# Performance work log

Hardware: AMD Instinct MI355X
Metric: run time of the kernel (lower is better)

## Reference

```python
import jax, jax.numpy as jnp
import numpy as np

N_NODES, N_EDGES, N_GRAPHS = 30000, 70000, 1024
TOWERS, F_IN, F_OUT, N_LAYERS = 5, 75, 15, 4
DEG_HIST = np.array([0.0, 100.0, 400.0, 300.0, 50.0], dtype=np.float32)
AVG_DEG_LOG = float((np.log(np.arange(len(DEG_HIST)) + 1.0) * DEG_HIST).sum() / DEG_HIST.sum())


def setup_inputs():
    key = jax.random.key(0)
    ks = jax.random.split(key, 16)
    g = lambda k, shp, fan: jax.random.normal(k, shp, jnp.float32) * (1.0 / np.sqrt(fan))
    return dict(
        x=jax.random.randint(ks[0], (N_NODES,), 0, 21),
        edge_index=jax.random.randint(ks[1], (2, N_EDGES), 0, N_NODES),
        edge_attr=jax.random.randint(ks[2], (N_EDGES,), 0, 4),
        batch=jnp.sort(jax.random.randint(ks[3], (N_NODES,), 0, N_GRAPHS)),
        node_emb=g(ks[4], (21, 75), 75),
        edge_emb=g(ks[5], (4, 50), 50),
        enc_w=g(ks[6], (N_LAYERS, 50, 75), 50),
        enc_b=jnp.zeros((N_LAYERS, 75), jnp.float32),
        pre_w=g(ks[7], (N_LAYERS, TOWERS, 3 * F_IN, F_IN), 3 * F_IN),
        pre_b=jnp.zeros((N_LAYERS, TOWERS, F_IN), jnp.float32),
        post_w=g(ks[8], (N_LAYERS, TOWERS, 13 * F_IN, F_OUT), 13 * F_IN),
        post_b=jnp.zeros((N_LAYERS, TOWERS, F_OUT), jnp.float32),
        lin_w=g(ks[9], (N_LAYERS, 75, 75), 75),
        lin_b=jnp.zeros((N_LAYERS, 75), jnp.float32),
        bn_g=jnp.ones((N_LAYERS, 75), jnp.float32),
        bn_b=jnp.zeros((N_LAYERS, 75), jnp.float32),
        mlp_w1=g(ks[10], (75, 50), 75), mlp_b1=jnp.zeros((50,), jnp.float32),
        mlp_w2=g(ks[11], (50, 25), 50), mlp_b2=jnp.zeros((25,), jnp.float32),
        mlp_w3=g(ks[12], (25, 1), 25), mlp_b3=jnp.zeros((1,), jnp.float32),
    )


def _pna_layer(h, src, dst, e_enc, pw, pb, qw, qb, lw, lb):
    n = h.shape[0]
    # message: cat[x_i, x_j, edge_enc] shared across towers, per-tower pre-NN
    msg = jnp.concatenate([h[dst], h[src], e_enc], axis=-1)            # [E, 3*F_in]
    m = jnp.einsum('ef,tfo->eto', msg, pw) + pb                        # [E, T, F_in]
    deg = jax.ops.segment_sum(jnp.ones((m.shape[0],), m.dtype), dst, n)
    has = (deg > 0)[:, None, None]
    cnt = jnp.maximum(deg, 1.0)[:, None, None]                         # clamp(1)
    mean = jax.ops.segment_sum(m, dst, n) / cnt
    mean_sq = jax.ops.segment_sum(m * m, dst, n) / cnt
    std = jnp.sqrt(jax.nn.relu(mean_sq - mean * mean) + 1e-5)
    mn = jnp.where(has, jax.ops.segment_min(m, dst, n), 0.0)
    mx = jnp.where(has, jax.ops.segment_max(m, dst, n), 0.0)
    agg = jnp.concatenate([mean, mn, mx, std], axis=-1)                # [N, T, 4*F_in]
    amp = jnp.log(cnt + 1.0) / AVG_DEG_LOG                             # amplification scaler
    scaled = jnp.concatenate([agg, agg * amp, agg / amp], axis=-1)     # [N, T, 12*F_in]
    post_in = jnp.concatenate(
        [jnp.broadcast_to(h[:, None, :], (n, TOWERS, F_IN)), scaled], axis=-1)  # [N, T, 13*F_in]
    out = jnp.einsum('ntf,tfo->nto', post_in, qw) + qb                 # [N, T, F_out]
    return out.reshape(n, TOWERS * F_OUT) @ lw + lb                    # [N, 75]


def _bn_relu(h, g, b):
    mu = h.mean(axis=0)
    var = h.var(axis=0)
    return jax.nn.relu((h - mu) * jax.lax.rsqrt(var + 1e-5) * g + b)


def reference(x, edge_index, edge_attr, batch, node_emb, edge_emb, enc_w, enc_b,
              pre_w, pre_b, post_w, post_b, lin_w, lin_b, bn_g, bn_b,
              mlp_w1, mlp_b1, mlp_w2, mlp_b2, mlp_w3, mlp_b3):
    h = node_emb[x]                      # [N, 75]
    e = edge_emb[edge_attr]              # [E, 50]
    src, dst = edge_index[0], edge_index[1]
    for l in range(N_LAYERS):
        e_enc = e @ enc_w[l] + enc_b[l]  # [E, 75]
        h = _bn_relu(_pna_layer(h, src, dst, e_enc, pre_w[l], pre_b[l],
                                post_w[l], post_b[l], lin_w[l], lin_b[l]),
                     bn_g[l], bn_b[l])
    hg = jax.ops.segment_sum(h, batch, N_GRAPHS)   # global_add_pool -> [G, 75]
    z = jax.nn.relu(hg @ mlp_w1 + mlp_b1)
    z = jax.nn.relu(z @ mlp_w2 + mlp_b2)
    return z @ mlp_w3 + mlp_b3
```

## Files before the change

### kernel.cpp

```cpp
#include <hip/hip_runtime.h>
#include <hip/hip_bf16.h>
#include <float.h>
#include <math.h>

#define NN 30000
#define NE 70000
#define NG 1024
#define NT 5
#define FI 75
#define NL 4

#define AMP_DENOM 1.1824939264481302f

#define ABW 832
#define AGW 1600
#define HBW 96
#define SBH 328

typedef __attribute__((ext_vector_type(8))) short bf16x8;
typedef __attribute__((ext_vector_type(4))) float f32x4;

__device__ __forceinline__ float bf2f(unsigned short u) {
    return __uint_as_float(((unsigned int)u) << 16);
}
__device__ __forceinline__ unsigned short f2bf(float f) {
    __hip_bfloat16 h = __float2bfloat16(f);
    return *reinterpret_cast<unsigned short*>(&h);
}

__global__ __launch_bounds__(256) void k_deg(const int* __restrict__ dst, int* __restrict__ deg) {
    int e = blockIdx.x * 256 + threadIdx.x;
    if (e < NE) atomicAdd(&deg[dst[e]], 1);
}

__global__ __launch_bounds__(1024) void k_scan(const int* __restrict__ deg, int* __restrict__ rowptr) {
    __shared__ int wsum[16];
    __shared__ int s_carry;
    int tid = threadIdx.x;
    int lane = tid & 63, wv = tid >> 6;
    if (tid == 0) s_carry = 0;
    __syncthreads();
    for (int base = 0; base < NN; base += 1024) {
        int i = base + tid;
        int v = (i < NN) ? deg[i] : 0;
        int x = v;
        #pragma unroll
        for (int off = 1; off < 64; off <<= 1) {
            int t = __shfl_up(x, off);
            if (lane >= off) x += t;
        }
        if (lane == 63) wsum[wv] = x;
        __syncthreads();
        if (tid < 16) {
            int y = wsum[tid];
            #pragma unroll
            for (int off = 1; off < 16; off <<= 1) {
                int t = __shfl_up(y, off);
                if (tid >= off) y += t;
            }
            wsum[tid] = y;
        }
        __syncthreads();
        int wbase = ((wv > 0) ? wsum[wv - 1] : 0) + s_carry;
        if (i < NN) rowptr[i] = wbase + x - v;
        int tot = wsum[15];
        __syncthreads();
        if (tid == 0) s_carry += tot;
    }
    __syncthreads();
    if (tid == 0) rowptr[NN] = s_carry;
}

__global__ __launch_bounds__(256) void k_scatter(const int* __restrict__ src, const int* __restrict__ dst,
                                                 const int* __restrict__ attr, const int* __restrict__ rowptr,
                                                 int* __restrict__ fill, int* __restrict__ csr) {
    int e = blockIdx.x * 256 + threadIdx.x;
    if (e < NE) {
        int d = dst[e];
        int pos = rowptr[d] + atomicAdd(&fill[d], 1);
        csr[pos] = src[e] | (attr[e] << 20);
    }
}

__global__ __launch_bounds__(256) void k_amp(const int* __restrict__ rowptr,
                                             float* __restrict__ amp, float* __restrict__ inv) {
    int n = blockIdx.x * 256 + threadIdx.x;
    if (n < NN) {
        int dg = rowptr[n + 1] - rowptr[n];
        float cnt = fmaxf((float)dg, 1.0f);
        float a = logf(cnt + 1.0f) * (1.0f / AMP_DENOM);
        amp[n] = a;
        inv[n] = 1.0f / a;
    }
}

__global__ __launch_bounds__(256) void k_h0(const int* __restrict__ x, const float* __restrict__ emb,
                                            float* __restrict__ h, unsigned short* __restrict__ hb) {
    int idx = blockIdx.x * 256 + threadIdx.x;
    if (idx < NN * HBW) {
        int n = idx / HBW, f = idx % HBW;
        if (f < FI) {
            float v = emb[x[n] * FI + f];
            h[n * FI + f] = v;
            hb[idx] = f2bf(v);
        } else {
            hb[idx] = 0;
        }
    }
}

__global__ __launch_bounds__(256) void k_wprep3(const float* __restrict__ post_w,
                                                unsigned short* __restrict__ Wpost2) {
    int idx = blockIdx.x * 256 + threadIdx.x;
    if (idx >= NL * NT * 3 * 16 * SBH) return;
    int kk = idx % SBH;
    int col = (idx / SBH) & 15;
    int s = (idx / (SBH * 16)) % 3;
    int t = (idx / (SBH * 16 * 3)) % NT;
    int l = idx / (SBH * 16 * 3 * NT);
    float val = 0.0f;
    if (kk < 304 && col < 15) {
        int stat = kk / 76, of = kk - stat * 76;
        if (of < 75)
            val = post_w[((size_t)(l * NT + t) * 975 + 75 + s * 300 + stat * 75 + of) * 15 + col];
    }
    Wpost2[idx] = f2bf(val);
}

__global__ __launch_bounds__(256) void k_wprep2(const float* __restrict__ pre_w,
                                                const float* __restrict__ post_w,
                                                unsigned short* __restrict__ WcatT) {
    int idx = blockIdx.x * 256 + threadIdx.x;
    if (idx >= NL * 832 * 96) return;
    int k = idx % 96;
    int j = (idx / 96) % 832;
    int l = idx / (96 * 832);
    float val = 0.0f;
    if (k < 75) {
        if (j < 375) {
            int t = j / 75, o = j % 75;
            val = pre_w[((size_t)(l * NT + t) * 225 + k) * FI + o];
        } else if (j < 750) {
            int jm = j - 375;
            int t = jm / 75, o = jm % 75;
            val = pre_w[((size_t)(l * NT + t) * 225 + 75 + k) * FI + o];
        } else if (j < 825) {
            int c = j - 750;
            int t = c / 15, o = c % 15;
            val = post_w[((size_t)(l * NT + t) * 975 + k) * 15 + o];
        }
    }
    WcatT[idx] = f2bf(val);
}

__global__ __launch_bounds__(384) void k_tbl(const float* __restrict__ edge_emb, const float* __restrict__ enc_w,
                                             const float* __restrict__ enc_b, const float* __restrict__ pre_w,
                                             const float* __restrict__ pre_b, int l,
                                             float* __restrict__ tbl, float* __restrict__ bnsum) {
    __shared__ float e4[4][FI];
    int tid = threadIdx.x;
    if (tid < 150) bnsum[tid] = 0.0f;
    if (tid < 300) {
        int a = tid / FI, f = tid % FI;
        float acc = enc_b[l * FI + f];
        for (int k = 0; k < 50; k++)
            acc += edge_emb[a * 50 + k] * enc_w[(l * 50 + k) * FI + f];
        e4[a][f] = acc;
    }
    __syncthreads();
    for (int idx = tid; idx < 4 * 375; idx += 384) {
        int a = idx / 375, c = idx % 375;
        int t = c / FI, o = c % FI;
        const float* wp = pre_w + ((size_t)(l * NT + t) * 225 + 150) * FI + o;
        float acc = pre_b[(l * NT + t) * FI + o];
        for (int f = 0; f < FI; f++)
            acc += e4[a][f] * wp[f * FI];
        tbl[idx] = acc;
    }
}

__global__ __launch_bounds__(256) void k_preab(const unsigned short* __restrict__ hb,
                                               const unsigned short* __restrict__ WcatT,
                                               int l, __hip_bfloat16* __restrict__ ABH) {
    __shared__ __align__(16) unsigned short sA[128 * 104];
    __shared__ __align__(16) unsigned short sB[208 * 104];
    int tid = threadIdx.x;
    int m0 = blockIdx.x * 128;
    int j0 = blockIdx.y * 208;

    const uint4* hsrc = (const uint4*)hb;
    for (int c = tid; c < 128 * 12; c += 256) {
        int r = c / 12, q = c % 12;
        int n = m0 + r;
        uint4 v = make_uint4(0, 0, 0, 0);
        if (n < NN) v = hsrc[(size_t)n * 12 + q];
        *(uint4*)&sA[r * 104 + q * 8] = v;
    }
    const uint4* wsrc = (const uint4*)(WcatT + (size_t)l * 832 * 96);
    for (int c = tid; c < 208 * 12; c += 256) {
        int r = c / 12, q = c % 12;
        *(uint4*)&sB[r * 104 + q * 8] = wsrc[(size_t)(j0 + r) * 12 + q];
    }
    __syncthreads();

    int w = tid >> 6, lane = tid & 63;
    int mw = w * 32;
    int lr = lane & 15, lq = lane >> 4;

    bf16x8 af[2][3];
    #pragma unroll
    for (int mt = 0; mt < 2; mt++)
        #pragma unroll
        for (int ks = 0; ks < 3; ks++)
            af[mt][ks] = *(const bf16x8*)&sA[(mw + mt * 16 + lr) * 104 + ks * 32 + lq * 8];

    f32x4 acc[13][2];
    #pragma unroll
    for (int nt = 0; nt < 13; nt++)
        #pragma unroll
        for (int mt = 0; mt < 2; mt++)
            acc[nt][mt] = (f32x4){0.0f, 0.0f, 0.0f, 0.0f};

    #pragma unroll
    for (int nt = 0; nt < 13; nt++) {
        #pragma unroll
        for (int ks = 0; ks < 3; ks++) {
            bf16x8 bf = *(const bf16x8*)&sB[(nt * 16 + lr) * 104 + ks * 32 + lq * 8];
            acc[nt][0] = __builtin_amdgcn_mfma_f32_16x16x32_bf16(af[0][ks], bf, acc[nt][0], 0, 0, 0);
            acc[nt][1] = __builtin_amdgcn_mfma_f32_16x16x32_bf16(af[1][ks], bf, acc[nt][1], 0, 0, 0);
        }
    }

    #pragma unroll
    for (int nt = 0; nt < 13; nt++) {
        int col = j0 + nt * 16 + lr;
        #pragma unroll
        for (int mt = 0; mt < 2; mt++) {
            #pragma unroll
            for (int r = 0; r < 4; r++) {
                int n = m0 + mw + mt * 16 + lq * 4 + r;
                if (n < NN) ABH[(size_t)n * ABW + col] = __float2bfloat16(acc[nt][mt][r]);
            }
        }
    }
}

__global__ __launch_bounds__(256) void k_gather(const __hip_bfloat16* __restrict__ ABH,
                                                const float* __restrict__ tbl,
                                                const int* __restrict__ rowptr, const int* __restrict__ csr,
                                                unsigned short* __restrict__ AGG) {
    __shared__ float s_tbl[1500];
    int tid = threadIdx.x;
    for (int i = tid; i < 1500; i += 256) s_tbl[i] = tbl[i];
    __syncthreads();

    int w = tid >> 6, l = tid & 63;
    int n = blockIdx.x * 4 + w;
    int base = rowptr[n];
    int dg = rowptr[n + 1] - base;

    float sum[6], ss[6], mn[6], mx[6];
    #pragma unroll
    for (int j = 0; j < 6; j++) { sum[j] = 0.f; ss[j] = 0.f; mn[j] = FLT_MAX; mx[j] = -FLT_MAX; }

    const unsigned short* abu = (const unsigned short*)ABH;
    for (int k = 0; k < dg; k++) {
        int pk = csr[base + k];
        int s = pk & 0xFFFFF;
        int a = pk >> 20;
        const unsigned short* bp = abu + (size_t)s * ABW + 375;
        const float* tp = s_tbl + a * 375;
        #pragma unroll
        for (int j = 0; j < 6; j++) {
            int f = l + 64 * j;
            if (f < 375) {
                float v = bf2f(bp[f]) + tp[f];
                sum[j] += v; ss[j] += v * v;
                mn[j] = fminf(mn[j], v); mx[j] = fmaxf(mx[j], v);
            }
        }
    }

    unsigned short* out = AGG + (size_t)n * AGW;
    if (dg > 0) {
        float rc = 1.0f / (float)dg;
        const unsigned short* ap = abu + (size_t)n * ABW;
        #pragma unroll
        for (int j = 0; j < 6; j++) {
            int f = l + 64 * j;
            if (f < 375) {
                int t = f / 75, of = f - t * 75;
                int o = t * 320 + of;
                float Af = bf2f(ap[f]);
                float mean = sum[j] * rc;
                float var = ss[j] * rc - mean * mean;
                out[o]       = f2bf(Af + mean);
                out[o + 76]  = f2bf(Af + mn[j]);
                out[o + 152] = f2bf(Af + mx[j]);
                out[o + 228] = f2bf(sqrtf(fmaxf(var, 0.0f) + 1e-5f));
            }
        }
    } else {
        unsigned short zz = 0;
        unsigned short sd = f2bf(0.0031622776601683794f);
        #pragma unroll
        for (int j = 0; j < 6; j++) {
            int f = l + 64 * j;
            if (f < 375) {
                int t = f / 75, of = f - t * 75;
                int o = t * 320 + of;
                out[o] = zz; out[o + 76] = zz; out[o + 152] = zz; out[o + 228] = sd;
            }
        }
    }
    for (int i = l; i < 80; i += 64) out[(i >> 4) * 320 + 304 + (i & 15)] = 0;
    if (l < 20) out[(l >> 2) * 320 + (l & 3) * 76 + 75] = 0;
}

__global__ __launch_bounds__(256) void k_post(const __hip_bfloat16* __restrict__ ABH,
                                              const unsigned short* __restrict__ AGG,
                                              const unsigned short* __restrict__ Wpost2,
                                              const float* __restrict__ amp_a, const float* __restrict__ inv_a,
                                              const float* __restrict__ post_b,
                                              const float* __restrict__ lin_w, const float* __restrict__ lin_b,
                                              int l, float* __restrict__ z, float* __restrict__ bnsum) {
    __shared__ __align__(16) float s_y[128 * 84];
    __shared__ __align__(16) unsigned short sB[3 * 16 * SBH];
    __shared__ float s_bn[152];

    int tid = threadIdx.x;
    int n0 = blockIdx.x * 128;
    int w = tid >> 6, lane = tid & 63;
    int lr = lane & 15, lq = lane >> 4;
    int mw = w * 32;
    if (tid < 152) s_bn[tid] = 0.0f;

    float am[2][4], iv[2][4];
    int rown[2][4];
    #pragma unroll
    for (int mt = 0; mt < 2; mt++)
        #pragma unroll
        for (int r = 0; r < 4; r++) {
            int n = n0 + mw + mt * 16 + lq * 4 + r;
            int nc = (n < NN) ? n : (NN - 1);
            rown[mt][r] = nc;
            am[mt][r] = amp_a[nc];
            iv[mt][r] = inv_a[nc];
        }
    int arow[2];
    #pragma unroll
    for (int mt = 0; mt < 2; mt++) {
        int n = n0 + mw + mt * 16 + lr;
        arow[mt] = (n < NN) ? n : (NN - 1);
    }

    const unsigned short* abu = (const unsigned short*)ABH;
    const unsigned short* wbase = Wpost2 + (size_t)l * NT * 3 * 16 * SBH;

    for (int t = 0; t < NT; t++) {
        __syncthreads();
        const uint4* gsrc = (const uint4*)(wbase + (size_t)t * 3 * 16 * SBH);
        uint4* gdst = (uint4*)sB;
        for (int i = tid; i < 3 * 16 * SBH / 8; i += 256) gdst[i] = gsrc[i];
        __syncthreads();

        f32x4 acc[2][3];
        #pragma unroll
        for (int mt = 0; mt < 2; mt++)
            #pragma unroll
            for (int s = 0; s < 3; s++)
                acc[mt][s] = (f32x4){0.0f, 0.0f, 0.0f, 0.0f};

        const unsigned short* a0p = AGG + (size_t)arow[0] * AGW + t * 320;
        const unsigned short* a1p = AGG + (size_t)arow[1] * AGW + t * 320;
        #pragma unroll
        for (int ks = 0; ks < 10; ks++) {
            int off = ks * 32 + lq * 8;
            bf16x8 b0 = *(const bf16x8*)&sB[0 * 16 * SBH + lr * SBH + off];
            bf16x8 b1 = *(const bf16x8*)&sB[1 * 16 * SBH + lr * SBH + off];
            bf16x8 b2 = *(const bf16x8*)&sB[2 * 16 * SBH + lr * SBH + off];
            bf16x8 a0 = *(const bf16x8*)&a0p[off];
            bf16x8 a1 = *(const bf16x8*)&a1p[off];
            acc[0][0] = __builtin_amdgcn_mfma_f32_16x16x32_bf16(a0, b0, acc[0][0], 0, 0, 0);
            acc[0][1] = __builtin_amdgcn_mfma_f32_16x16x32_bf16(a0, b1, acc[0][1], 0, 0, 0);
            acc[0][2] = __builtin_amdgcn_mfma_f32_16x16x32_bf16(a0, b2, acc[0][2], 0, 0, 0);
            acc[1][0] = __builtin_amdgcn_mfma_f32_16x16x32_bf16(a1, b0, acc[1][0], 0, 0, 0);
            acc[1][1] = __builtin_amdgcn_mfma_f32_16x16x32_bf16(a1, b1, acc[1][1], 0, 0, 0);
            acc[1][2] = __builtin_amdgcn_mfma_f32_16x16x32_bf16(a1, b2, acc[1][2], 0, 0, 0);
        }

        if (lr < 15) {
            float qb = post_b[(l * NT + t) * 15 + lr];
            #pragma unroll
            for (int mt = 0; mt < 2; mt++)
                #pragma unroll
                for (int r = 0; r < 4; r++) {
                    float ht = bf2f(abu[(size_t)rown[mt][r] * ABW + 750 + t * 15 + lr]);
                    float y = acc[mt][0][r] + am[mt][r] * acc[mt][1][r] + iv[mt][r] * acc[mt][2][r] + ht + qb;
                    s_y[(mw + mt * 16 + lq * 4 + r) * 84 + t * 15 + lr] = y;
                }
        }
    }
    __syncthreads();

    float* s_lw = (float*)sB;
    for (int i = tid; i < 5625; i += 256) {
        int k = i / 75, c = i - k * 75;
        s_lw[k * 80 + c] = lin_w[(size_t)l * 5625 + i];
    }
    __syncthreads();

    int tx = tid & 15, ty = tid >> 4;
    float acc2[8][5];
    #pragma unroll
    for (int r = 0; r < 8; r++)
        #pragma unroll
        for (int u = 0; u < 5; u++) {
            int c = tx + 16 * u;
            acc2[r][u] = (c < 75) ? lin_b[l * 75 + c] : 0.0f;
        }
    for (int k = 0; k < 75; k++) {
        float wv[5];
        #pragma unroll
        for (int u = 0; u < 5; u++) {
            int c = tx + 16 * u;
            wv[u] = (c < 75) ? s_lw[k * 80 + c] : 0.0f;
        }
        #pragma unroll
        for (int r = 0; r < 8; r++) {
            float yv = s_y[(ty + r * 16) * 84 + k];
            #pragma unroll
            for (int u = 0; u < 5; u++) acc2[r][u] += yv * wv[u];
        }
    }

    float b1a[5] = {}, b2a[5] = {};
    #pragma unroll
    for (int r = 0; r < 8; r++) {
        int n = n0 + ty + r * 16;
        bool nv = (n < NN);
        #pragma unroll
        for (int u = 0; u < 5; u++) {
            int c = tx + 16 * u;
            if (c < 75 && nv) {
                z[(size_t)n * 75 + c] = acc2[r][u];
                b1a[u] += acc2[r][u];
                b2a[u] += acc2[r][u] * acc2[r][u];
            }
        }
    }
    #pragma unroll
    for (int u = 0; u < 5; u++) {
        b1a[u] += __shfl_xor(b1a[u], 16); b1a[u] += __shfl_xor(b1a[u], 32);
        b2a[u] += __shfl_xor(b2a[u], 16); b2a[u] += __shfl_xor(b2a[u], 32);
    }
    if ((tid & 63) < 16) {
        #pragma unroll
        for (int u = 0; u < 5; u++) {
            int c = tx + 16 * u;
            if (c < 75) {
                atomicAdd(&s_bn[c], b1a[u]);
                atomicAdd(&s_bn[76 + c], b2a[u]);
            }
        }
    }
    __syncthreads();
    if (tid < 75) {
        atomicAdd(&bnsum[tid], s_bn[tid]);
        atomicAdd(&bnsum[75 + tid], s_bn[76 + tid]);
    }
}

__global__ __launch_bounds__(256) void k_bn(const float* __restrict__ z, const float* __restrict__ bnsum,
                                            const float* __restrict__ bn_g, const float* __restrict__ bn_b,
                                            int l, float* __restrict__ h, unsigned short* __restrict__ hb) {
    int idx = blockIdx.x * 256 + threadIdx.x;
    if (idx < NN * 75) {
        int n = idx / 75, c = idx % 75;
        float mu = bnsum[c] * (1.0f / NN);
        float msq = bnsum[75 + c] * (1.0f / NN);
        float var = msq - mu * mu;
        float v = (z[idx] - mu) * rsqrtf(var + 1e-5f) * bn_g[l * 75 + c] + bn_b[l * 75 + c];
        v = fmaxf(v, 0.0f);
        h[idx] = v;
        hb[n * HBW + c] = f2bf(v);
    }
}

__global__ __launch_bounds__(256) void k_pool(const float* __restrict__ h, const int* __restrict__ batch,
                                              float* __restrict__ hg) {
    int idx = blockIdx.x * 256 + threadIdx.x;
    if (idx < NN * 75) {
        int n = idx / 75, f = idx % 75;
        atomicAdd(&hg[batch[n] * 75 + f], h[idx]);
    }
}

__global__ __launch_bounds__(64) void k_mlp(const float* __restrict__ hg,
                                            const float* __restrict__ w1, const float* __restrict__ b1,
                                            const float* __restrict__ w2, const float* __restrict__ b2,
                                            const float* __restrict__ w3, const float* __restrict__ b3,
                                            float* __restrict__ out) {
    __shared__ float zin[75], z1[50], z2[25];
    int g = blockIdx.x, tid = threadIdx.x;
    for (int k = tid; k < 75; k += 64) zin[k] = hg[g * 75 + k];
    __syncthreads();
    if (tid < 50) {
        float acc = b1[tid];
        for (int k = 0; k < 75; k++) acc += zin[k] * w1[k * 50 + tid];
        z1[tid] = fmaxf(acc, 0.0f);
    }
    __syncthreads();
    if (tid < 25) {
        float acc = b2[tid];
        for (int k = 0; k < 50; k++) acc += z1[k] * w2[k * 25 + tid];
        z2[tid] = fmaxf(acc, 0.0f);
    }
    __syncthreads();
    if (tid == 0) {
        float acc = b3[0];
        for (int k = 0; k < 25; k++) acc += z2[k] * w3[k];
        out[g] = acc;
    }
}

extern "C" void kernel_launch(void* const* d_in, const int* in_sizes, int n_in,
                              void* d_out, int out_size, void* d_ws, size_t ws_size,
                              hipStream_t stream) {
    const int* x        = (const int*)d_in[0];
    const int* ei       = (const int*)d_in[1];
    const int* eattr    = (const int*)d_in[2];
    const int* batch    = (const int*)d_in[3];
    const float* node_emb = (const float*)d_in[4];
    const float* edge_emb = (const float*)d_in[5];
    const float* enc_w  = (const float*)d_in[6];
    const float* enc_b  = (const float*)d_in[7];
    const float* pre_w  = (const float*)d_in[8];
    const float* pre_b  = (const float*)d_in[9];
    const float* post_w = (const float*)d_in[10];
    const float* post_b = (const float*)d_in[11];
    const float* lin_w  = (const float*)d_in[12];
    const float* lin_b  = (const float*)d_in[13];
    const float* bn_g   = (const float*)d_in[14];
    const float* bn_b   = (const float*)d_in[15];
    const float* w1     = (const float*)d_in[16];
    const float* b1     = (const float*)d_in[17];
    const float* w2     = (const float*)d_in[18];
    const float* b2     = (const float*)d_in[19];
    const float* w3     = (const float*)d_in[20];
    const float* b3     = (const float*)d_in[21];

    char* p = (char*)d_ws;
    auto carve = [&](size_t bytes) -> char* {
        char* r = p;
        p += ((bytes + 255) & ~(size_t)255);
        return r;
    };
    __hip_bfloat16* ABH = (__hip_bfloat16*)carve((size_t)NN * ABW * 2);
    unsigned short* AGG = (unsigned short*)carve((size_t)NN * AGW * 2);
    float* h     = (float*)carve((size_t)NN * 75 * 4);
    float* z     = (float*)carve((size_t)NN * 75 * 4);
    unsigned short* hb = (unsigned short*)carve((size_t)NN * HBW * 2);
    unsigned short* WcatT = (unsigned short*)carve((size_t)NL * 832 * 96 * 2);
    unsigned short* Wpost2 = (unsigned short*)carve((size_t)NL * NT * 3 * 16 * SBH * 2);
    float* tbl   = (float*)carve(1500 * 4);
    int* deg     = (int*)carve(NN * 4);
    int* rowptr  = (int*)carve((NN + 1) * 4);
    int* fill    = (int*)carve(NN * 4);
    int* csr     = (int*)carve(NE * 4);
    float* bnsum = (float*)carve(150 * 4);
    float* amp_a = (float*)carve(NN * 4);
    float* inv_a = (float*)carve(NN * 4);
    float* hg    = (float*)carve((size_t)NG * 75 * 4);

    hipMemsetAsync(deg, 0, NN * 4, stream);
    hipMemsetAsync(fill, 0, NN * 4, stream);
    hipMemsetAsync(hg, 0, (size_t)NG * 75 * 4, stream);

    k_deg<<<(NE + 255) / 256, 256, 0, stream>>>(ei + NE, deg);
    k_scan<<<1, 1024, 0, stream>>>(deg, rowptr);
    k_scatter<<<(NE + 255) / 256, 256, 0, stream>>>(ei, ei + NE, eattr, rowptr, fill, csr);
    k_amp<<<(NN + 255) / 256, 256, 0, stream>>>(rowptr, amp_a, inv_a);
    k_h0<<<(NN * HBW + 255) / 256, 256, 0, stream>>>(x, node_emb, h, hb);
    k_wprep3<<<(NL * NT * 3 * 16 * SBH + 255) / 256, 256, 0, stream>>>(post_w, Wpost2);
    k_wprep2<<<(NL * 832 * 96 + 255) / 256, 256, 0, stream>>>(pre_w, post_w, WcatT);

    for (int l = 0; l < NL; l++) {
        k_tbl<<<1, 384, 0, stream>>>(edge_emb, enc_w, enc_b, pre_w, pre_b, l, tbl, bnsum);
        k_preab<<<dim3((NN + 127) / 128, 4), 256, 0, stream>>>(hb, WcatT, l, ABH);
        k_gather<<<NN / 4, 256, 0, stream>>>(ABH, tbl, rowptr, csr, AGG);
        k_post<<<(NN + 127) / 128, 256, 0, stream>>>(ABH, AGG, Wpost2, amp_a, inv_a,
                                                     post_b, lin_w, lin_b, l, z, bnsum);
        k_bn<<<(NN * 75 + 255) / 256, 256, 0, stream>>>(z, bnsum, bn_g, bn_b, l, h, hb);
    }

    k_pool<<<(NN * 75 + 255) / 256, 256, 0, stream>>>(h, batch, hg);
    k_mlp<<<NG, 64, 0, stream>>>(hg, w1, b1, w2, b2, w3, b3, (float*)d_out);
}
```

Before: 589.7 us.

## Fuse batchnorm into next layer, MFMA lin projection, hoist edge tables

Removes the separate batchnorm kernel: the BN+ReLU apply now happens while loading z in the next layer's pre-projection GEMM and inside the final pooling kernel, with per-layer BN sums kept in separate buffers. The final 75x75 linear layer in k_post is moved from scalar FMA to bf16 MFMA using a pretransposed weight, and post weights are read directly from global memory instead of being staged in LDS. Edge-attribute tables for all layers are precomputed once up front, and the gather loop is unrolled by two edges. This cuts kernel launches and one full pass over z/h each layer, but adds bf16 rounding of the intermediate y and more global weight reads.

```diff
diff --git a/kernel.cpp b/kernel.cpp
--- a/kernel.cpp
+++ b/kernel.cpp
@@ -95,17 +95,11 @@
 }
 
 __global__ __launch_bounds__(256) void k_h0(const int* __restrict__ x, const float* __restrict__ emb,
-                                            float* __restrict__ h, unsigned short* __restrict__ hb) {
+                                            unsigned short* __restrict__ hb) {
     int idx = blockIdx.x * 256 + threadIdx.x;
     if (idx < NN * HBW) {
         int n = idx / HBW, f = idx % HBW;
-        if (f < FI) {
-            float v = emb[x[n] * FI + f];
-            h[n * FI + f] = v;
-            hb[idx] = f2bf(v);
-        } else {
-            hb[idx] = 0;
-        }
+        hb[idx] = (f < FI) ? f2bf(emb[x[n] * FI + f]) : (unsigned short)0;
     }
 }
 
@@ -153,13 +147,25 @@
     WcatT[idx] = f2bf(val);
 }
 
-__global__ __launch_bounds__(384) void k_tbl(const float* __restrict__ edge_emb, const float* __restrict__ enc_w,
-                                             const float* __restrict__ enc_b, const float* __restrict__ pre_w,
-                                             const float* __restrict__ pre_b, int l,
-                                             float* __restrict__ tbl, float* __restrict__ bnsum) {
+__global__ __launch_bounds__(256) void k_wprep4(const float* __restrict__ lin_w,
+                                                unsigned short* __restrict__ linT) {
+    int idx = blockIdx.x * 256 + threadIdx.x;
+    if (idx >= NL * 80 * 96) return;
+    int k = idx % 96;
+    int c = (idx / 96) % 80;
+    int l = idx / (96 * 80);
+    float v = 0.0f;
+    if (k < 75 && c < 75) v = lin_w[(size_t)l * 5625 + k * 75 + c];
+    linT[idx] = f2bf(v);
+}
+
+__global__ __launch_bounds__(384) void k_tbl4(const float* __restrict__ edge_emb, const float* __restrict__ enc_w,
+                                              const float* __restrict__ enc_b, const float* __restrict__ pre_w,
+                                              const float* __restrict__ pre_b, float* __restrict__ tbl4) {
     __shared__ float e4[4][FI];
+    int l = blockIdx.x;
     int tid = threadIdx.x;
-    if (tid < 150) bnsum[tid] = 0.0f;
+    float* tbl = tbl4 + l * 1500;
     if (tid < 300) {
         int a = tid / FI, f = tid % FI;
         float acc = enc_b[l * FI + f];
@@ -180,26 +186,53 @@
 }
 
 __global__ __launch_bounds__(256) void k_preab(const unsigned short* __restrict__ hb,
+                                               const float* __restrict__ zz,
+                                               const float* __restrict__ bnsumP,
+                                               const float* __restrict__ bngP,
+                                               const float* __restrict__ bnbP,
                                                const unsigned short* __restrict__ WcatT,
                                                int l, __hip_bfloat16* __restrict__ ABH) {
     __shared__ __align__(16) unsigned short sA[128 * 104];
     __shared__ __align__(16) unsigned short sB[208 * 104];
+    __shared__ float s_sc[75], s_sh[75];
     int tid = threadIdx.x;
     int m0 = blockIdx.x * 128;
     int j0 = blockIdx.y * 208;
 
-    const uint4* hsrc = (const uint4*)hb;
-    for (int c = tid; c < 128 * 12; c += 256) {
-        int r = c / 12, q = c % 12;
-        int n = m0 + r;
-        uint4 v = make_uint4(0, 0, 0, 0);
-        if (n < NN) v = hsrc[(size_t)n * 12 + q];
-        *(uint4*)&sA[r * 104 + q * 8] = v;
+    if (l > 0 && tid < 75) {
+        float mu = bnsumP[tid] * (1.0f / NN);
+        float msq = bnsumP[76 + tid] * (1.0f / NN);
+        float var = msq - mu * mu;
+        float sc = rsqrtf(var + 1e-5f) * bngP[tid];
+        s_sc[tid] = sc;
+        s_sh[tid] = bnbP[tid] - mu * sc;
     }
     const uint4* wsrc = (const uint4*)(WcatT + (size_t)l * 832 * 96);
     for (int c = tid; c < 208 * 12; c += 256) {
         int r = c / 12, q = c % 12;
         *(uint4*)&sB[r * 104 + q * 8] = wsrc[(size_t)(j0 + r) * 12 + q];
+    }
+    if (l == 0) {
+        const uint4* hsrc = (const uint4*)hb;
+        for (int c = tid; c < 128 * 12; c += 256) {
+            int r = c / 12, q = c % 12;
+            int n = m0 + r;
+            uint4 v = make_uint4(0, 0, 0, 0);
+            if (n < NN) v = hsrc[(size_t)n * 12 + q];
+            *(uint4*)&sA[r * 104 + q * 8] = v;
+        }
+    } else {
+        __syncthreads();
+        for (int idx = tid; idx < 128 * 96; idx += 256) {
+            int r = idx / 96, c = idx - (idx / 96) * 96;
+            int n = m0 + r;
+            float v = 0.0f;
+            if (c < 75 && n < NN) {
+                v = zz[(size_t)n * 75 + c];
+                v = fmaxf(v * s_sc[c] + s_sh[c], 0.0f);
+            }
+            sA[r * 104 + c] = f2bf(v);
+        }
     }
     __syncthreads();
 
@@ -264,19 +297,37 @@
     for (int j = 0; j < 6; j++) { sum[j] = 0.f; ss[j] = 0.f; mn[j] = FLT_MAX; mx[j] = -FLT_MAX; }
 
     const unsigned short* abu = (const unsigned short*)ABH;
-    for (int k = 0; k < dg; k++) {
-        int pk = csr[base + k];
-        int s = pk & 0xFFFFF;
-        int a = pk >> 20;
-        const unsigned short* bp = abu + (size_t)s * ABW + 375;
-        const float* tp = s_tbl + a * 375;
+    int k = 0;
+    for (; k + 1 < dg; k += 2) {
+        int pk0 = csr[base + k], pk1 = csr[base + k + 1];
+        const unsigned short* bp0 = abu + (size_t)(pk0 & 0xFFFFF) * ABW + 375;
+        const unsigned short* bp1 = abu + (size_t)(pk1 & 0xFFFFF) * ABW + 375;
+        const float* tp0 = s_tbl + (pk0 >> 20) * 375;
+        const float* tp1 = s_tbl + (pk1 >> 20) * 375;
         #pragma unroll
         for (int j = 0; j < 6; j++) {
             int f = l + 64 * j;
             if (f < 375) {
-                float v = bf2f(bp[f]) + tp[f];
-                sum[j] += v; ss[j] += v * v;
-                mn[j] = fminf(mn[j], v); mx[j] = fmaxf(mx[j], v);
+                float v0 = bf2f(bp0[f]) + tp0[f];
+                float v1 = bf2f(bp1[f]) + tp1[f];
+                sum[j] += v0 + v1;
+                ss[j] += v0 * v0 + v1 * v1;
+                mn[j] = fminf(mn[j], fminf(v0, v1));
+                mx[j] = fmaxf(mx[j], fmaxf(v0, v1));
+            }
+        }
+    }
+    if (k < dg) {
+        int pk0 = csr[base + k];
+        const unsigned short* bp0 = abu + (size_t)(pk0 & 0xFFFFF) * ABW + 375;
+        const float* tp0 = s_tbl + (pk0 >> 20) * 375;
+        #pragma unroll
+        for (int j = 0; j < 6; j++) {
+            int f = l + 64 * j;
+            if (f < 375) {
+                float v0 = bf2f(bp0[f]) + tp0[f];
+                sum[j] += v0; ss[j] += v0 * v0;
+                mn[j] = fminf(mn[j], v0); mx[j] = fmaxf(mx[j], v0);
             }
         }
     }
@@ -320,12 +371,11 @@
 __global__ __launch_bounds__(256) void k_post(const __hip_bfloat16* __restrict__ ABH,
                                               const unsigned short* __restrict__ AGG,
                                               const unsigned short* __restrict__ Wpost2,
+                                              const unsigned short* __restrict__ linT,
                                               const float* __restrict__ amp_a, const float* __restrict__ inv_a,
-                                              const float* __restrict__ post_b,
-                                              const float* __restrict__ lin_w, const float* __restrict__ lin_b,
+                                              const float* __restrict__ post_b, const float* __restrict__ lin_b,
                                               int l, float* __restrict__ z, float* __restrict__ bnsum) {
-    __shared__ __align__(16) float s_y[128 * 84];
-    __shared__ __align__(16) unsigned short sB[3 * 16 * SBH];
+    __shared__ __align__(16) unsigned short s_y[128 * 96];
     __shared__ float s_bn[152];
 
     int tid = threadIdx.x;
@@ -334,6 +384,10 @@
     int lr = lane & 15, lq = lane >> 4;
     int mw = w * 32;
     if (tid < 152) s_bn[tid] = 0.0f;
+    for (int i = tid; i < 128 * 21; i += 256) {
+        int r = i / 21, c = 75 + (i - (i / 21) * 21);
+        s_y[r * 96 + c] = 0;
+    }
 
     float am[2][4], iv[2][4];
     int rown[2][4];
@@ -355,14 +409,11 @@
     }
 
     const unsigned short* abu = (const unsigned short*)ABH;
-    const unsigned short* wbase = Wpost2 + (size_t)l * NT * 3 * 16 * SBH;
 
     for (int t = 0; t < NT; t++) {
-        __syncthreads();
-        const uint4* gsrc = (const uint4*)(wbase + (size_t)t * 3 * 16 * SBH);
-        uint4* gdst = (uint4*)sB;
-        for (int i = tid; i < 3 * 16 * SBH / 8; i += 256) gdst[i] = gsrc[i];
-        __syncthreads();
+        const unsigned short* wt = Wpost2 + ((size_t)((l * NT + t) * 3 * 16) + lr) * SBH;
+        const unsigned short* a0p = AGG + (size_t)arow[0] * AGW + t * 320;
+        const unsigned short* a1p = AGG + (size_t)arow[1] * AGW + t * 320;
 
         f32x4 acc[2][3];
         #pragma unroll
@@ -371,14 +422,12 @@
             for (int s = 0; s < 3; s++)
                 acc[mt][s] = (f32x4){0.0f, 0.0f, 0.0f, 0.0f};
 
-        const unsigned short* a0p = AGG + (size_t)arow[0] * AGW + t * 320;
-        const unsigned short* a1p = AGG + (size_t)arow[1] * AGW + t * 320;
         #pragma unroll
         for (int ks = 0; ks < 10; ks++) {
             int off = ks * 32 + lq * 8;
-            bf16x8 b0 = *(const bf16x8*)&sB[0 * 16 * SBH + lr * SBH + off];
-            bf16x8 b1 = *(const bf16x8*)&sB[1 * 16 * SBH + lr * SBH + off];
-            bf16x8 b2 = *(const bf16x8*)&sB[2 * 16 * SBH + lr * SBH + off];
+            bf16x8 b0 = *(const bf16x8*)&wt[off];
+            bf16x8 b1 = *(const bf16x8*)&wt[16 * SBH + off];
+            bf16x8 b2 = *(const bf16x8*)&wt[32 * SBH + off];
             bf16x8 a0 = *(const bf16x8*)&a0p[off];
             bf16x8 a1 = *(const bf16x8*)&a1p[off];
             acc[0][0] = __builtin_amdgcn_mfma_f32_16x16x32_bf16(a0, b0, acc[0][0], 0, 0, 0);
@@ -397,102 +446,97 @@
                 for (int r = 0; r < 4; r++) {
                     float ht = bf2f(abu[(size_t)rown[mt][r] * ABW + 750 + t * 15 + lr]);
                     float y = acc[mt][0][r] + am[mt][r] * acc[mt][1][r] + iv[mt][r] * acc[mt][2][r] + ht + qb;
-                    s_y[(mw + mt * 16 + lq * 4 + r) * 84 + t * 15 + lr] = y;
+                    s_y[(mw + mt * 16 + lq * 4 + r) * 96 + t * 15 + lr] = f2bf(y);
                 }
         }
     }
     __syncthreads();
 
-    float* s_lw = (float*)sB;
-    for (int i = tid; i < 5625; i += 256) {
-        int k = i / 75, c = i - k * 75;
-        s_lw[k * 80 + c] = lin_w[(size_t)l * 5625 + i];
-    }
-    __syncthreads();
-
-    int tx = tid & 15, ty = tid >> 4;
-    float acc2[8][5];
-    #pragma unroll
-    for (int r = 0; r < 8; r++)
-        #pragma unroll
-        for (int u = 0; u < 5; u++) {
-            int c = tx + 16 * u;
-            acc2[r][u] = (c < 75) ? lin_b[l * 75 + c] : 0.0f;
-        }
-    for (int k = 0; k < 75; k++) {
-        float wv[5];
-        #pragma unroll
-        for (int u = 0; u < 5; u++) {
-            int c = tx + 16 * u;
-            wv[u] = (c < 75) ? s_lw[k * 80 + c] : 0.0f;
-        }
-        #pragma unroll
-        for (int r = 0; r < 8; r++) {
-            float yv = s_y[(ty + r * 16) * 84 + k];
+    const unsigned short* lt = linT + (size_t)l * 80 * 96;
+    bf16x8 af[2][3];
+    #pragma unroll
+    for (int mt = 0; mt < 2; mt++)
+        #pragma unroll
+        for (int ks = 0; ks < 3; ks++)
+            af[mt][ks] = *(const bf16x8*)&s_y[(mw + mt * 16 + lr) * 96 + ks * 32 + lq * 8];
+
+    f32x4 acc2[5][2];
+    #pragma unroll
+    for (int nt = 0; nt < 5; nt++)
+        #pragma unroll
+        for (int mt = 0; mt < 2; mt++)
+            acc2[nt][mt] = (f32x4){0.0f, 0.0f, 0.0f, 0.0f};
+
+    #pragma unroll
+    for (int nt = 0; nt < 5; nt++) {
+        #pragma unroll
+        for (int ks = 0; ks < 3; ks++) {
+            bf16x8 bf = *(const bf16x8*)&lt[(nt * 16 + lr) * 96 + ks * 32 + lq * 8];
+            acc2[nt][0] = __builtin_amdgcn_mfma_f32_16x16x32_bf16(af[0][ks], bf, acc2[nt][0], 0, 0, 0);
+            acc2[nt][1] = __builtin_amdgcn_mfma_f32_16x16x32_bf16(af[1][ks], bf, acc2[nt][1], 0, 0, 0);
+        }
+    }
+
+    float b1a[5] = {}, b2a[5] = {};
+    #pragma unroll
+    for (int nt = 0; nt < 5; nt++) {
+        int c = nt * 16 + lr;
+        bool cv = (c < 75);
+        float lb = cv ? lin_b[l * 75 + c] : 0.0f;
+        #pragma unroll
+        for (int mt = 0; mt < 2; mt++)
             #pragma unroll
-            for (int u = 0; u < 5; u++) acc2[r][u] += yv * wv[u];
-        }
-    }
-
-    float b1a[5] = {}, b2a[5] = {};
-    #pragma unroll
-    for (int r = 0; r < 8; r++) {
-        int n = n0 + ty + r * 16;
-        bool nv = (n < NN);
-        #pragma unroll
-        for (int u = 0; u < 5; u++) {
-            int c = tx + 16 * u;
-            if (c < 75 && nv) {
-                z[(size_t)n * 75 + c] = acc2[r][u];
-                b1a[u] += acc2[r][u];
-                b2a[u] += acc2[r][u] * acc2[r][u];
-            }
-        }
-    }
-    #pragma unroll
-    for (int u = 0; u < 5; u++) {
-        b1a[u] += __shfl_xor(b1a[u], 16); b1a[u] += __shfl_xor(b1a[u], 32);
-        b2a[u] += __shfl_xor(b2a[u], 16); b2a[u] += __shfl_xor(b2a[u], 32);
-    }
-    if ((tid & 63) < 16) {
-        #pragma unroll
-        for (int u = 0; u < 5; u++) {
-            int c = tx + 16 * u;
+            for (int r = 0; r < 4; r++) {
+                int n = n0 + mw + mt * 16 + lq * 4 + r;
+                if (cv && n < NN) {
+                    float v = acc2[nt][mt][r] + lb;
+                    z[(size_t)n * 75 + c] = v;
+                    b1a[nt] += v;
+                    b2a[nt] += v * v;
+                }
+            }
+    }
+    #pragma unroll
+    for (int nt = 0; nt < 5; nt++) {
+        b1a[nt] += __shfl_xor(b1a[nt], 16); b1a[nt] += __shfl_xor(b1a[nt], 32);
+        b2a[nt] += __shfl_xor(b2a[nt], 16); b2a[nt] += __shfl_xor(b2a[nt], 32);
+    }
+    if (lq == 0) {
+        #pragma unroll
+        for (int nt = 0; nt < 5; nt++) {
+            int c = nt * 16 + lr;
             if (c < 75) {
-                atomicAdd(&s_bn[c], b1a[u]);
-                atomicAdd(&s_bn[76 + c], b2a[u]);
+                atomicAdd(&s_bn[c], b1a[nt]);
+                atomicAdd(&s_bn[76 + c], b2a[nt]);
             }
         }
     }
     __syncthreads();
     if (tid < 75) {
         atomicAdd(&bnsum[tid], s_bn[tid]);
-        atomicAdd(&bnsum[75 + tid], s_bn[76 + tid]);
-    }
-}
-
-__global__ __launch_bounds__(256) void k_bn(const float* __restrict__ z, const float* __restrict__ bnsum,
-                                            const float* __restrict__ bn_g, const float* __restrict__ bn_b,
-                                            int l, float* __restrict__ h, unsigned short* __restrict__ hb) {
-    int idx = blockIdx.x * 256 + threadIdx.x;
-    if (idx < NN * 75) {
-        int n = idx / 75, c = idx % 75;
-        float mu = bnsum[c] * (1.0f / NN);
-        float msq = bnsum[75 + c] * (1.0f / NN);
+        atomicAdd(&bnsum[76 + tid], s_bn[76 + tid]);
+    }
+}
+
+__global__ __launch_bounds__(256) void k_pool(const float* __restrict__ z, const float* __restrict__ bnsum3,
+                                              const float* __restrict__ bng, const float* __restrict__ bnb,
+                                              const int* __restrict__ batch, float* __restrict__ hg) {
+    __shared__ float s_sc[75], s_sh[75];
+    int tid = threadIdx.x;
+    if (tid < 75) {
+        float mu = bnsum3[tid] * (1.0f / NN);
+        float msq = bnsum3[76 + tid] * (1.0f / NN);
         float var = msq - mu * mu;
-        float v = (z[idx] - mu) * rsqrtf(var + 1e-5f) * bn_g[l * 75 + c] + bn_b[l * 75 + c];
-        v = fmaxf(v, 0.0f);
-        h[idx] = v;
-        hb[n * HBW + c] = f2bf(v);
-    }
-}
-
-__global__ __launch_bounds__(256) void k_pool(const float* __restrict__ h, const int* __restrict__ batch,
-                                              float* __restrict__ hg) {
-    int idx = blockIdx.x * 256 + threadIdx.x;
+        float sc = rsqrtf(var + 1e-5f) * bng[tid];
+        s_sc[tid] = sc;
+        s_sh[tid] = bnb[tid] - mu * sc;
+    }
+    __syncthreads();
+    int idx = blockIdx.x * 256 + tid;
     if (idx < NN * 75) {
         int n = idx / 75, f = idx % 75;
-        atomicAdd(&hg[batch[n] * 75 + f], h[idx]);
+        float v = fmaxf(z[idx] * s_sc[f] + s_sh[f], 0.0f);
+        atomicAdd(&hg[batch[n] * 75 + f], v);
     }
 }
 
@@ -558,17 +602,17 @@
     };
     __hip_bfloat16* ABH = (__hip_bfloat16*)carve((size_t)NN * ABW * 2);
     unsigned short* AGG = (unsigned short*)carve((size_t)NN * AGW * 2);
-    float* h     = (float*)carve((size_t)NN * 75 * 4);
     float* z     = (float*)carve((size_t)NN * 75 * 4);
     unsigned short* hb = (unsigned short*)carve((size_t)NN * HBW * 2);
     unsigned short* WcatT = (unsigned short*)carve((size_t)NL * 832 * 96 * 2);
     unsigned short* Wpost2 = (unsigned short*)carve((size_t)NL * NT * 3 * 16 * SBH * 2);
-    float* tbl   = (float*)carve(1500 * 4);
+    unsigned short* linT = (unsigned short*)carve((size_t)NL * 80 * 96 * 2);
+    float* tbl4  = (float*)carve((size_t)NL * 1500 * 4);
     int* deg     = (int*)carve(NN * 4);
     int* rowptr  = (int*)carve((NN + 1) * 4);
     int* fill    = (int*)carve(NN * 4);
     int* csr     = (int*)carve(NE * 4);
-    float* bnsum = (float*)carve(150 * 4);
+    float* bnsum = (float*)carve((size_t)NL * 152 * 4);
     float* amp_a = (float*)carve(NN * 4);
     float* inv_a = (float*)carve(NN * 4);
     float* hg    = (float*)carve((size_t)NG * 75 * 4);
@@ -576,24 +620,29 @@
     hipMemsetAsync(deg, 0, NN * 4, stream);
     hipMemsetAsync(fill, 0, NN * 4, stream);
     hipMemsetAsync(hg, 0, (size_t)NG * 75 * 4, stream);
+    hipMemsetAsync(bnsum, 0, (size_t)NL * 152 * 4, stream);
 
     k_deg<<<(NE + 255) / 256, 256, 0, stream>>>(ei + NE, deg);
     k_scan<<<1, 1024, 0, stream>>>(deg, rowptr);
     k_scatter<<<(NE + 255) / 256, 256, 0, stream>>>(ei, ei + NE, eattr, rowptr, fill, csr);
     k_amp<<<(NN + 255) / 256, 256, 0, stream>>>(rowptr, amp_a, inv_a);
-    k_h0<<<(NN * HBW + 255) / 256, 256, 0, stream>>>(x, node_emb, h, hb);
+    k_h0<<<(NN * HBW + 255) / 256, 256, 0, stream>>>(x, node_emb, hb);
     k_wprep3<<<(NL * NT * 3 * 16 * SBH + 255) / 256, 256, 0, stream>>>(post_w, Wpost2);
     k_wprep2<<<(NL * 832 * 96 + 255) / 256, 256, 0, stream>>>(pre_w, post_w, WcatT);
+    k_wprep4<<<(NL * 80 * 96 + 255) / 256, 256, 0, stream>>>(lin_w, linT);
+    k_tbl4<<<NL, 384, 0, stream>>>(edge_emb, enc_w, enc_b, pre_w, pre_b, tbl4);
 
     for (int l = 0; l < NL; l++) {
-        k_tbl<<<1, 384, 0, stream>>>(edge_emb, enc_w, enc_b, pre_w, pre_b, l, tbl, bnsum);
-        k_preab<<<dim3((NN + 127) / 128, 4), 256, 0, stream>>>(hb, WcatT, l, ABH);
-        k_gather<<<NN / 4, 256, 0, stream>>>(ABH, tbl, rowptr, csr, AGG);
-        k_post<<<(NN + 127) / 128, 256, 0, stream>>>(ABH, AGG, Wpost2, amp_a, inv_a,
-                                                     post_b, lin_w, lin_b, l, z, bnsum);
-        k_bn<<<(NN * 75 + 255) / 256, 256, 0, stream>>>(z, bnsum, bn_g, bn_b, l, h, hb);
-    }
-
-    k_pool<<<(NN * 75 + 255) / 256, 256, 0, stream>>>(h, batch, hg);
+        k_preab<<<dim3((NN + 127) / 128, 4), 256, 0, stream>>>(
+            hb, z, bnsum + (l > 0 ? (l - 1) * 152 : 0),
+            bn_g + (l > 0 ? (l - 1) * 75 : 0), bn_b + (l > 0 ? (l - 1) * 75 : 0),
+            WcatT, l, ABH);
+        k_gather<<<NN / 4, 256, 0, stream>>>(ABH, tbl4 + l * 1500, rowptr, csr, AGG);
+        k_post<<<(NN + 127) / 128, 256, 0, stream>>>(ABH, AGG, Wpost2, linT, amp_a, inv_a,
+                                                     post_b, lin_b, l, z, bnsum + l * 152);
+    }
+
+    k_pool<<<(NN * 75 + 255) / 256, 256, 0, stream>>>(z, bnsum + 3 * 152, bn_g + 3 * 75, bn_b + 3 * 75,
+                                                      batch, hg);
     k_mlp<<<NG, 64, 0, stream>>>(hg, w1, b1, w2, b2, w3, b3, (float*)d_out);
 }
```

Result: no change. 583.1 us (-1.1%).
